# Kernel tuning notes

Hardware: AMD Instinct MI355X
Metric: run time of the kernel (lower is better)

## Reference

```python
import jax, jax.numpy as jnp
import numpy as np

D_MODEL = 192; D_INNER = 384; N_STATE = 16; D_CONV = 4; DT_RANK = 12; DEPTH = 24
PATCH = 16; STRIDE = 16; IMG = 128; EPS = 1e-5


def _ln(x, w, b):
    m = jnp.mean(x, -1, keepdims=True)
    v = jnp.mean((x - m) ** 2, -1, keepdims=True)
    return (x - m) * jax.lax.rsqrt(v + EPS) * w + b


def _mamba_dir(xz, cw, cb, xpw, dpw, dpb, Alog, Dv):
    # xz: (B, L, 2*d_inner); one direction of the bidirectional Mamba mixer
    xp, z = jnp.split(xz, 2, axis=-1)               # (B,L,di) each
    xc = jnp.transpose(xp, (0, 2, 1))               # (B,di,L)
    xc = jnp.pad(xc, ((0, 0), (0, 0), (D_CONV - 1, 0)))  # causal pad
    xc = jax.lax.conv_general_dilated(
        xc, cw, (1,), 'VALID',
        dimension_numbers=('NCH', 'OIH', 'NCH'),
        feature_group_count=D_INNER) + cb[None, :, None]
    u = jax.nn.silu(jnp.transpose(xc, (0, 2, 1)))   # (B,L,di)
    dbl = u @ xpw.T                                  # (B,L,dt_rank+2N)
    dt, Bm, Cm = jnp.split(dbl, [DT_RANK, DT_RANK + N_STATE], axis=-1)
    dt = jax.nn.softplus(dt @ dpw.T + dpb)           # (B,L,di)
    A = -jnp.exp(Alog)                               # (di,N)
    dA = jnp.exp(dt[..., None] * A)                  # (B,L,di,N)
    dBu = (dt * u)[..., None] * Bm[:, :, None, :]    # (B,L,di,N)

    def comb(c1, c2):
        a1, b1 = c1
        a2, b2 = c2
        return a1 * a2, a2 * b1 + b2

    _, h = jax.lax.associative_scan(comb, (dA, dBu), axis=1)
    y = jnp.einsum('bldn,bln->bld', h, Cm) + u * Dv
    return y * jax.nn.silu(z)


def _forward(x, patch_w, patch_b, ln_w, ln_b, in_w,
             cf_w, cf_b, xpf_w, dtf_w, dtf_b, Alog_f, D_f,
             cbk_w, cbk_b, xpb_w, dtb_w, dtb_b, Alog_b, D_b,
             out_w, nf_w, nf_b, head_w, head_b):
    B = x.shape[0]
    p = jax.lax.conv_general_dilated(
        x, patch_w, (STRIDE,) * 3, 'VALID',
        dimension_numbers=('NCDHW', 'OIDHW', 'NCDHW')) + patch_b[None, :, None, None, None]
    hidden = p.reshape(B, D_MODEL, -1).transpose(0, 2, 1)  # (B, L=512, D)
    residual = jnp.zeros_like(hidden)

    xs = (ln_w, ln_b, in_w, cf_w, cf_b, xpf_w, dtf_w, dtf_b, Alog_f, D_f,
          cbk_w, cbk_b, xpb_w, dtb_w, dtb_b, Alog_b, D_b, out_w)

    def step(carry, pl):
        hidden, residual = carry
        (lw, lb, iw, cfw, cfb, xpf, dwf, dbf, Af, Dfv,
         cbw, cbb, xpb, dwb, dbb, Ab, Dbv, ow) = pl
        residual = residual + hidden
        hn = _ln(residual, lw, lb)
        xz = hn @ iw.T                               # (B,L,2di)
        yf = _mamba_dir(xz, cfw, cfb, xpf, dwf, dbf, Af, Dfv)
        yb = jnp.flip(_mamba_dir(jnp.flip(xz, 1), cbw, cbb, xpb, dwb, dbb, Ab, Dbv), 1)
        hidden = (yf + yb) @ ow.T
        return (hidden, residual), None

    (hidden, residual), _ = jax.lax.scan(step, (hidden, residual), xs)
    final = _ln(residual + hidden, nf_w, nf_b)
    feat = final[:, -1, :]                           # final_pool_type='none' -> last token
    return feat @ head_w.T + head_b


def setup_inputs() -> dict:
    key = jax.random.key(0)
    ks = jax.random.split(key, 16)
    rn = lambda k, s, sc=0.02: jax.random.normal(k, s, jnp.float32) * sc
    d = {}
    d['x'] = jax.random.normal(ks[0], (1, 1, IMG, IMG, IMG), jnp.float32)
    d['patch_w'] = rn(ks[1], (D_MODEL, 1, PATCH, PATCH, PATCH), 0.05)
    d['patch_b'] = jnp.zeros((D_MODEL,), jnp.float32)
    d['ln_w'] = jnp.ones((DEPTH, D_MODEL), jnp.float32)
    d['ln_b'] = jnp.zeros((DEPTH, D_MODEL), jnp.float32)
    d['in_w'] = rn(ks[2], (DEPTH, 2 * D_INNER, D_MODEL))
    d['cf_w'] = rn(ks[3], (DEPTH, D_INNER, 1, D_CONV), 0.2)
    d['cf_b'] = jnp.zeros((DEPTH, D_INNER), jnp.float32)
    d['xpf_w'] = rn(ks[4], (DEPTH, DT_RANK + 2 * N_STATE, D_INNER))
    d['dtf_w'] = rn(ks[5], (DEPTH, D_INNER, DT_RANK), 0.1)
    d['dtf_b'] = jnp.full((DEPTH, D_INNER), -4.6, jnp.float32)  # softplus -> dt~0.01
    d['Alog_f'] = jnp.log(jnp.broadcast_to(jnp.arange(1, N_STATE + 1, dtype=jnp.float32), (DEPTH, D_INNER, N_STATE)))
    d['D_f'] = jnp.ones((DEPTH, D_INNER), jnp.float32)
    d['cbk_w'] = rn(ks[6], (DEPTH, D_INNER, 1, D_CONV), 0.2)
    d['cbk_b'] = jnp.zeros((DEPTH, D_INNER), jnp.float32)
    d['xpb_w'] = rn(ks[7], (DEPTH, DT_RANK + 2 * N_STATE, D_INNER))
    d['dtb_w'] = rn(ks[8], (DEPTH, D_INNER, DT_RANK), 0.1)
    d['dtb_b'] = jnp.full((DEPTH, D_INNER), -4.6, jnp.float32)
    d['Alog_b'] = jnp.log(jnp.broadcast_to(jnp.arange(1, N_STATE + 1, dtype=jnp.float32), (DEPTH, D_INNER, N_STATE)))
    d['D_b'] = jnp.ones((DEPTH, D_INNER), jnp.float32)
    d['out_w'] = rn(ks[9], (DEPTH, D_MODEL, D_INNER))
    d['nf_w'] = jnp.ones((D_MODEL,), jnp.float32)
    d['nf_b'] = jnp.zeros((D_MODEL,), jnp.float32)
    d['head_w'] = rn(ks[10], (2, D_MODEL))
    d['head_b'] = jnp.zeros((2,), jnp.float32)
    return d


def reference(x, patch_w, patch_b, ln_w, ln_b, in_w,
              cf_w, cf_b, xpf_w, dtf_w, dtf_b, Alog_f, D_f,
              cbk_w, cbk_b, xpb_w, dtb_w, dtb_b, Alog_b, D_b,
              out_w, nf_w, nf_b, head_w, head_b):
    return _forward(x, patch_w, patch_b, ln_w, ln_b, in_w,
                    cf_w, cf_b, xpf_w, dtf_w, dtf_b, Alog_f, D_f,
                    cbk_w, cbk_b, xpb_w, dtb_w, dtb_b, Alog_b, D_b,
                    out_w, nf_w, nf_b, head_w, head_b)
```

## Files before the change

### kernel.cpp

```cpp
#include <hip/hip_runtime.h>
#include <hip/hip_bf16.h>

#define D_MODEL 192
#define D_INNER 384
#define N_STATE 16
#define DT_RANK 12
#define DEPTH 24
#define SEQ 512
#define NCHUNK 8
#define CLEN 64
#define TS 68
#define AS 33
#define PART_STRIDE (SEQ * D_MODEL)
#define USTR (SEQ * D_INNER)
#define KSPLIT 16
#define NBLK 1024
#define FSTR 32
#define XZSTR (SEQ * 2 * D_INNER)
#define CHSTR (2 * NCHUNK * D_INNER * N_STATE)
#define GEN_OFF   1024
#define SCANR_OFF 1056
#define AFLAG_OFF 1440
#define BFLAG_OFF 1952
#define YFLAG_OFF 2976

typedef __hip_bfloat16 bf16;
typedef unsigned short u16;
typedef unsigned long long u64;

__device__ __forceinline__ float silu_f(float x) { return x / (1.f + __expf(-x)); }
__device__ __forceinline__ float softplus_f(float x) {
    return (x > 20.f) ? x : log1pf(__expf(x));
}
__device__ __forceinline__ float bf2f(unsigned u) {
    return __uint_as_float(u << 16);
}
__device__ __forceinline__ u16 f2bu(float f) {
    bf16 b = __float2bfloat16(f);
    return *reinterpret_cast<u16*>(&b);
}

__device__ __forceinline__ float aload(const float* p) {
    return __hip_atomic_load(p, __ATOMIC_RELAXED, __HIP_MEMORY_SCOPE_AGENT);
}
__device__ __forceinline__ void astore(float* p, float v) {
    __hip_atomic_store(p, v, __ATOMIC_RELAXED, __HIP_MEMORY_SCOPE_AGENT);
}
__device__ __forceinline__ unsigned aloadu(const unsigned* p) {
    return __hip_atomic_load(p, __ATOMIC_RELAXED, __HIP_MEMORY_SCOPE_AGENT);
}
__device__ __forceinline__ void astoreu(unsigned* p, unsigned v) {
    __hip_atomic_store(p, v, __ATOMIC_RELAXED, __HIP_MEMORY_SCOPE_AGENT);
}
__device__ __forceinline__ float2 aload2(const float* p) {
    const u64 v = __hip_atomic_load((const u64*)p, __ATOMIC_RELAXED, __HIP_MEMORY_SCOPE_AGENT);
    return make_float2(__uint_as_float((unsigned)v), __uint_as_float((unsigned)(v >> 32)));
}
__device__ __forceinline__ void astore2(float* p, float x, float y) {
    const u64 v = (u64)__float_as_uint(x) | ((u64)__float_as_uint(y) << 32);
    __hip_atomic_store((u64*)p, v, __ATOMIC_RELAXED, __HIP_MEMORY_SCOPE_AGENT);
}
__device__ __forceinline__ float4 aload4v(const float* p) {
    const float2 a = aload2(p), b = aload2(p + 2);
    return make_float4(a.x, a.y, b.x, b.y);
}
__device__ __forceinline__ float4 aload_bf4(const u16* p) {
    const u64 v = __hip_atomic_load((const u64*)p, __ATOMIC_RELAXED, __HIP_MEMORY_SCOPE_AGENT);
    return make_float4(bf2f((unsigned)(v & 0xffffu)),
                       bf2f((unsigned)((v >> 16) & 0xffffu)),
                       bf2f((unsigned)((v >> 32) & 0xffffu)),
                       bf2f((unsigned)(v >> 48)));
}
__device__ __forceinline__ void astore_bf4(u16* p, float a, float b, float c, float d) {
    const u64 v = (u64)f2bu(a) | ((u64)f2bu(b) << 16)
                | ((u64)f2bu(c) << 32) | ((u64)f2bu(d) << 48);
    __hip_atomic_store((u64*)p, v, __ATOMIC_RELAXED, __HIP_MEMORY_SCOPE_AGENT);
}

template<typename T> __device__ __forceinline__ float ld(const void* p, long i) {
    return ((const float*)p)[i];
}
template<> __device__ __forceinline__ float ld<bf16>(const void* p, long i) {
    return bf2f(((const u16*)p)[i]);
}
template<typename T> __device__ __forceinline__ float4 ld4(const void* p, long i) {
    return *(const float4*)((const float*)p + i);
}
template<> __device__ __forceinline__ float4 ld4<bf16>(const void* p, long i) {
    const ushort4 v = *(const ushort4*)((const u16*)p + i);
    return make_float4(bf2f(v.x), bf2f(v.y), bf2f(v.z), bf2f(v.w));
}
template<typename T> __device__ __forceinline__ void st(void* p, int i, float v) {
    ((float*)p)[i] = v;
}
template<> __device__ __forceinline__ void st<bf16>(void* p, int i, float v) {
    ((bf16*)p)[i] = __float2bfloat16(v);
}
__device__ __forceinline__ float dot4(const float4& a, const float4& b) {
    return a.x * b.x + a.y * b.y + a.z * b.z + a.w * b.w;
}
__device__ __forceinline__ void ld8b(const u16* p, float4& a, float4& b) {
    const uint4 u = *(const uint4*)p;
    a.x = bf2f(u.x & 0xffffu); a.y = bf2f(u.x >> 16);
    a.z = bf2f(u.y & 0xffffu); a.w = bf2f(u.y >> 16);
    b.x = bf2f(u.z & 0xffffu); b.y = bf2f(u.z >> 16);
    b.z = bf2f(u.w & 0xffffu); b.w = bf2f(u.w >> 16);
}
__device__ __forceinline__ float4 ld4b(const u16* p) {
    const uint2 u = *(const uint2*)p;
    return make_float4(bf2f(u.x & 0xffffu), bf2f(u.x >> 16),
                       bf2f(u.y & 0xffffu), bf2f(u.y >> 16));
}

__device__ __forceinline__ void post_flag(unsigned* fl, unsigned v, int tid) {
    asm volatile("s_waitcnt vmcnt(0)" ::: "memory");
    __syncthreads();
    if (tid == 0) astoreu(fl, v);
}
__device__ __forceinline__ void wait_flag(const unsigned* fl, unsigned v) {
    int spins = 0;
    while (aloadu(fl) < v) {
        if (++spins > (1 << 20)) break;
        __builtin_amdgcn_s_sleep(1);
    }
}

__device__ __forceinline__ void gbar(unsigned* bar, unsigned target, bool fence) {
    asm volatile("s_waitcnt vmcnt(0)" ::: "memory");
    __syncthreads();
    const int bid = blockIdx.x, tid = threadIdx.x;
    unsigned* gen0 = bar + GEN_OFF * FSTR;
    if (tid == 0) {
        if (fence) __threadfence();
        astoreu(&bar[bid * FSTR], target);
    }
    if (bid == 0) {
        int spins = 0;
        for (;;) {
            const unsigned va = aloadu(&bar[tid * FSTR]);
            const unsigned vb = aloadu(&bar[(tid + 256) * FSTR]);
            const unsigned vc = aloadu(&bar[(tid + 512) * FSTR]);
            const unsigned vd = aloadu(&bar[(tid + 768) * FSTR]);
            const bool ok = (va >= target) && (vb >= target) && (vc >= target) && (vd >= target);
            if (__syncthreads_and(ok)) break;
            if (++spins > (1 << 20)) break;
            __builtin_amdgcn_s_sleep(1);
        }
        if (tid == 0) astoreu(gen0, target);
    } else if (tid == 0) {
        int spins = 0;
        if (bid < 32) {
            while (aloadu(gen0) < target) {
                if (++spins > (1 << 20)) break;
                __builtin_amdgcn_s_sleep(2);
            }
            astoreu(&gen0[bid * FSTR], target);
        } else {
            unsigned* rl = &gen0[(bid >> 5) * FSTR];
            while (aloadu(rl) < target) {
                if (++spins > (1 << 20)) break;
                __builtin_amdgcn_s_sleep(2);
            }
        }
    }
    if (fence && tid == 0) __threadfence();
    __syncthreads();
}

__device__ void cvtB(const void* s, u16* d, long n, long g, long str, int isb) {
    if (isb) {
        const u16* p = (const u16*)s;
        for (long i = g * 4; i < n; i += str * 4) *(ushort4*)(d + i) = *(const ushort4*)(p + i);
    } else {
        const float* p = (const float*)s;
        for (long i = g * 4; i < n; i += str * 4) {
            const float4 v = *(const float4*)(p + i);
            ushort4 o; o.x = f2bu(v.x); o.y = f2bu(v.y); o.z = f2bu(v.z); o.w = f2bu(v.w);
            *(ushort4*)(d + i) = o;
        }
    }
}
__device__ void cvtF(const void* s, float* d, long n, long g, long str, int isb) {
    if (isb) {
        const u16* p = (const u16*)s;
        for (long i = g * 4; i < n; i += str * 4) {
            const ushort4 v = *(const ushort4*)(p + i);
            *(float4*)(d + i) = make_float4(bf2f(v.x), bf2f(v.y), bf2f(v.z), bf2f(v.w));
        }
    } else {
        const float* p = (const float*)s;
        for (long i = g * 4; i < n; i += str * 4) *(float4*)(d + i) = *(const float4*)(p + i);
    }
}
__device__ void cvtNA(const void* s, float* d, long n, long g, long str, int isb) {
    if (isb) {
        const u16* p = (const u16*)s;
        for (long i = g * 4; i < n; i += str * 4) {
            const ushort4 v = *(const ushort4*)(p + i);
            *(float4*)(d + i) = make_float4(-__expf(bf2f(v.x)), -__expf(bf2f(v.y)),
                                            -__expf(bf2f(v.z)), -__expf(bf2f(v.w)));
        }
    } else {
        const float* p = (const float*)s;
        for (long i = g * 4; i < n; i += str * 4) {
            const float4 v = *(const float4*)(p + i);
            *(float4*)(d + i) = make_float4(-__expf(v.x), -__expf(v.y), -__expf(v.z), -__expf(v.w));
        }
    }
}

template<typename T>
__device__ void final_phase(int tid, const float* res, const u16* yB, const void* ow,
                            const void* nw, const void* nb, const void* hw, const void* hb,
                            void* out, float* syf, float* f, float* red) {
    for (int j = tid; j < 96; j += 256) {
        const int q = j * 4;
        const float4 vf = aload_bf4(&yB[(long)511 * D_INNER + q]);
        const float4 vb = aload_bf4(&yB[(long)USTR + 511 * D_INNER + q]);
        *(float4*)&syf[q] = make_float4(vf.x + vb.x, vf.y + vb.y, vf.z + vb.z, vf.w + vb.w);
    }
    __syncthreads();
    float v = 0.f;
    if (tid < D_MODEL) {
        float acc = 0.f;
        const long wrow = (long)(DEPTH - 1) * D_MODEL * D_INNER + (long)tid * D_INNER;
        for (int k = 0; k < D_INNER; k += 4)
            acc += dot4(ld4<T>(ow, wrow + k), *(const float4*)&syf[k]);
        v = aload(&res[511 * D_MODEL + tid]) + acc;
    }
    float s = v;
    #pragma unroll
    for (int o = 32; o > 0; o >>= 1) s += __shfl_down(s, o, 64);
    if ((tid & 63) == 0 && tid < D_MODEL) red[tid >> 6] = s;
    __syncthreads();
    const float mean = (red[0] + red[1] + red[2]) * (1.f / D_MODEL);
    const float d = (tid < D_MODEL) ? (v - mean) : 0.f;
    float s2 = d * d;
    #pragma unroll
    for (int o = 32; o > 0; o >>= 1) s2 += __shfl_down(s2, o, 64);
    if ((tid & 63) == 0 && tid < D_MODEL) red[3 + (tid >> 6)] = s2;
    __syncthreads();
    const float var = (red[3] + red[4] + red[5]) * (1.f / D_MODEL);
    if (tid < D_MODEL)
        f[tid] = d * rsqrtf(var + 1e-5f) * ld<T>(nw, tid) + ld<T>(nb, tid);
    __syncthreads();
    if (tid < 2) {
        float a2 = ld<T>(hb, tid);
        for (int c = 0; c < D_MODEL; ++c) a2 += f[c] * ld<T>(hw, tid * D_MODEL + c);
        st<T>(out, tid, a2);
    }
}

struct MegaArgs {
    const void *x, *pw, *pb, *lnw, *lnb, *inw, *cfw, *cfb, *xpfw, *dtfw, *dtfb, *Af, *Dfv;
    const void *cbw, *cbb, *xpbw, *dtbw, *dtbb, *Ab, *Dbv, *ow, *nfw, *nfb, *hw, *hb;
    void* out;
    unsigned* bar;
    float *hidC, *res0, *res1, *dbl, *dt, *chunkH, *chunkP;
    u16 *xzB, *uB, *yB;
    float *lnwF, *lnbF, *cbfF, *cbbF, *dtbfF, *dtbbF, *negAfF, *negAbF, *DfF, *DbF, *pbF;
    u16 *inwB, *owB, *xB, *pwB, *xpwfB, *xpwbB, *dtwfB, *dtwbB, *cwfB, *cwbB;
};

__global__ void init_kernel(unsigned* bar) {
    const int i = blockIdx.x * 256 + threadIdx.x;
    ((uint4*)bar)[i] = make_uint4(0, 0, 0, 0);
}

__global__ void __launch_bounds__(256, 4) mega_kernel(MegaArgs a) {
    __shared__ float smem[6144];
    const int bid = blockIdx.x;
    const int tid = threadIdx.x;
    unsigned* bar = a.bar;
    unsigned* scanR = a.bar + SCANR_OFF * FSTR;
    unsigned* aflag = a.bar + AFLAG_OFF * FSTR;
    unsigned* bflag = a.bar + BFLAG_OFF * FSTR;
    unsigned* yflag = a.bar + YFLAG_OFF * FSTR;
    unsigned gen_ctr = 0;
    const int isb = (((const unsigned*)a.lnw)[0] != 0x3F800000u);

    {
        const long g = (long)bid * 256 + tid;
        const long str = (long)NBLK * 256;
        cvtB(a.inw,  a.inwB,  3538944, g, str, isb);
        cvtB(a.ow,   a.owB,   1769472, g, str, isb);
        cvtB(a.x,    a.xB,    2097152, g, str, isb);
        cvtB(a.pw,   a.pwB,    786432, g, str, isb);
        cvtB(a.xpfw, a.xpwfB,  405504, g, str, isb);
        cvtB(a.xpbw, a.xpwbB,  405504, g, str, isb);
        cvtB(a.dtfw, a.dtwfB,  110592, g, str, isb);
        cvtB(a.dtbw, a.dtwbB,  110592, g, str, isb);
        cvtB(a.cfw,  a.cwfB,    36864, g, str, isb);
        cvtB(a.cbw,  a.cwbB,    36864, g, str, isb);
        cvtF(a.lnw,  a.lnwF,     4608, g, str, isb);
        cvtF(a.lnb,  a.lnbF,     4608, g, str, isb);
        cvtF(a.cfb,  a.cbfF,     9216, g, str, isb);
        cvtF(a.cbb,  a.cbbF,     9216, g, str, isb);
        cvtF(a.dtfb, a.dtbfF,    9216, g, str, isb);
        cvtF(a.dtbb, a.dtbbF,    9216, g, str, isb);
        cvtF(a.pb,   a.pbF,       192, g, str, isb);
        cvtNA(a.Af,  a.negAfF,  147456, g, str, isb);
        cvtNA(a.Ab,  a.negAbF,  147456, g, str, isb);
        cvtF(a.Dfv,  a.DfF,      9216, g, str, isb);
        cvtF(a.Dbv,  a.DbF,      9216, g, str, isb);
    }
    gbar(bar, ++gen_ctr, true);

    if (bid < 768) {
        float* As_ = smem;
        float* Ws  = smem + 1056;
        const int ty = tid >> 4, tx = tid & 15;
        const int unit = bid;
        {
            const int mt = unit & 15, nt = (unit >> 4) % 3, ks = unit / 48;
            const int m0 = mt * 32, n0 = nt * 64, kk0 = ks * 256;
            float acc[2][4] = {};
            for (int kk = kk0; kk < kk0 + 256; kk += 32) {
                for (int e = tid; e < 1024; e += 256) {
                    const int m = e >> 5, k = e & 31;
                    const int kid = kk + k, t = m0 + m;
                    const int dz = kid >> 8, dy = (kid >> 4) & 15, dx = kid & 15;
                    const int pz = t >> 6, py = (t >> 3) & 7, px = t & 7;
                    As_[k * AS + m] = bf2f(a.xB[(long)(pz * 16 + dz) * 16384 + (py * 16 + dy) * 128 + (px * 16 + dx)]);
                }
                for (int e = tid; e < 2048; e += 256) {
                    const int n = e >> 5, k = e & 31;
                    Ws[k * TS + n] = bf2f(a.pwB[(long)(n0 + n) * 4096 + kk + k]);
                }
                __syncthreads();
                #pragma unroll 8
                for (int k = 0; k < 32; ++k) {
                    const float a0 = As_[k * AS + ty * 2];
                    const float a1 = As_[k * AS + ty * 2 + 1];
                    const float4 w4 = *(const float4*)&Ws[k * TS + tx * 4];
                    acc[0][0] += a0 * w4.x; acc[0][1] += a0 * w4.y;
                    acc[0][2] += a0 * w4.z; acc[0][3] += a0 * w4.w;
                    acc[1][0] += a1 * w4.x; acc[1][1] += a1 * w4.y;
                    acc[1][2] += a1 * w4.z; acc[1][3] += a1 * w4.w;
                }
                __syncthreads();
            }
            float* C = a.hidC + (long)ks * PART_STRIDE;
            #pragma unroll
            for (int i = 0; i < 2; ++i) {
                float4 o4 = make_float4(acc[i][0], acc[i][1], acc[i][2], acc[i][3]);
                if (ks == 0) {
                    o4.x += a.pbF[n0 + tx * 4 + 0];
                    o4.y += a.pbF[n0 + tx * 4 + 1];
                    o4.z += a.pbF[n0 + tx * 4 + 2];
                    o4.w += a.pbF[n0 + tx * 4 + 3];
                }
                astore2(&C[(m0 + ty * 2 + i) * D_MODEL + n0 + tx * 4], o4.x, o4.y);
                astore2(&C[(m0 + ty * 2 + i) * D_MODEL + n0 + tx * 4 + 2], o4.z, o4.w);
            }
        }
    }
    gbar(bar, ++gen_ctr, false);

    const int ch = tid >> 4, np = tid & 15;
    float* sU  = smem;
    float* sDT = smem + 1024;
    float* sBC = smem + 2048;
    float* sZ  = smem + 4096;
    float* sY  = smem + 5120;

    for (int l = 0; l < DEPTH; ++l) {
        const int first = (l == 0);
        const unsigned lv = (unsigned)(l + 1);
        const int par = l & 1;
        u16* xzP = a.xzB + (long)par * XZSTR;
        u16* uP  = a.uB  + (long)par * (2 * USTR);
        float* dtP = a.dt + (long)par * (2 * USTR);
        float* dbG = a.dbl + (long)par * (2 * SEQ * 44);
        float* chH = a.chunkH + (long)par * CHSTR;
        float* chPb = a.chunkP + (long)par * CHSTR;
        const float* resIn = par ? a.res1 : a.res0;
        float* resOut      = par ? a.res0 : a.res1;

        if (bid < 512) {
            const int t = bid;
            if (par) {
                if (tid < 48) {
                    const int dd = tid / 24, dg = tid - dd * 24;
                    const int cf = t >> 6;
                    const int cbk = (511 - t) >> 6;
                    const int cc = dd ? cbk : cf;
                    wait_flag(&yflag[((dd * NCHUNK + cc) * 24 + dg) * FSTR], (unsigned)l);
                }
                __syncthreads();
            }
            float* sy  = smem;
            float* lnS = smem + 384;
            float* hnS = smem + 576;
            float* xzS = smem + 768;
            if (!first && tid < 96) {
                const int q4 = tid * 4;
                const long o = (long)t * D_INNER + q4;
                const float4 vf = aload_bf4(&a.yB[o]);
                const float4 vb = aload_bf4(&a.yB[(long)USTR + o]);
                *(float4*)&sy[q4] = make_float4(vf.x + vb.x, vf.y + vb.y, vf.z + vb.z, vf.w + vb.w);
            }
            __syncthreads();
            if (tid < D_MODEL) {
                float acc;
                if (first) {
                    float s = 0.f;
                    #pragma unroll
                    for (int sp = 0; sp < KSPLIT; ++sp)
                        s += aload(&a.hidC[(long)sp * PART_STRIDE + t * D_MODEL + tid]);
                    acc = s;
                } else {
                    acc = 0.f;
                    const u16* wr = a.owB + (long)(l - 1) * D_MODEL * D_INNER + (long)tid * D_INNER;
                    for (int k = 0; k < D_INNER; k += 8) {
                        float4 va, vb;
                        ld8b(wr + k, va, vb);
                        acc += dot4(va, *(const float4*)&sy[k]) + dot4(vb, *(const float4*)&sy[k + 4]);
                    }
                }
                const float rv = acc + (first ? 0.f : aload(&resIn[t * D_MODEL + tid]));
                lnS[tid] = rv;
                astore(&resOut[t * D_MODEL + tid], rv);
            }
            __syncthreads();
            {
                const int w = tid >> 6, lane = tid & 63;
                if (w == 0) {
                    const float v0 = lnS[lane];
                    const float v1 = lnS[lane + 64];
                    const float v2 = lnS[lane + 128];
                    float s = v0 + v1 + v2;
                    #pragma unroll
                    for (int o = 32; o > 0; o >>= 1) s += __shfl_xor(s, o, 64);
                    const float mean = s * (1.f / D_MODEL);
                    const float d0 = v0 - mean, d1 = v1 - mean, d2 = v2 - mean;
                    float s2 = d0 * d0 + d1 * d1 + d2 * d2;
                    #pragma unroll
                    for (int o = 32; o > 0; o >>= 1) s2 += __shfl_xor(s2, o, 64);
                    const float rstd = rsqrtf(s2 * (1.f / D_MODEL) + 1e-5f);
                    hnS[lane]       = d0 * rstd * a.lnwF[l * D_MODEL + lane]       + a.lnbF[l * D_MODEL + lane];
                    hnS[lane + 64]  = d1 * rstd * a.lnwF[l * D_MODEL + lane + 64]  + a.lnbF[l * D_MODEL + lane + 64];
                    hnS[lane + 128] = d2 * rstd * a.lnwF[l * D_MODEL + lane + 128] + a.lnbF[l * D_MODEL + lane + 128];
                }
            }
            __syncthreads();
            float accD[3] = {};
            const u16* w0 = a.inwB + (long)l * 2 * D_INNER * D_MODEL;
            for (int k = 0; k < D_MODEL; k += 8) {
                #pragma unroll
                for (int r = 0; r < 3; ++r) {
                    float4 va, vb;
                    ld8b(w0 + (long)(tid + r * 256) * D_MODEL + k, va, vb);
                    accD[r] += dot4(va, *(const float4*)&hnS[k])
                             + dot4(vb, *(const float4*)&hnS[k + 4]);
                }
            }
            #pragma unroll
            for (int r = 0; r < 3; ++r) xzS[tid + r * 256] = accD[r];
            __syncthreads();
            if (tid < 192) {
                const int q = tid * 4;
                const float* s = &xzS[q];
                astore_bf4(&xzP[(long)t * 2 * D_INNER + q], s[0], s[1], s[2], s[3]);
            }
            post_flag(&aflag[t * FSTR], lv, tid);
        }

        {
            const int dir = bid >> 9, t = bid & 511;
            int lo, hi;
            if (dir == 0) { lo = t >= 3 ? t - 3 : 0; hi = t; }
            else { lo = 508 - t >= 0 ? 508 - t : 0; hi = 511 - t; }
            if (tid <= hi - lo) wait_flag(&aflag[(lo + tid) * FSTR], lv);
            __syncthreads();

            float* su   = smem;
            float* dblP = smem + 384;
            float* dblS = smem + 472;
            const u16* cwB   = dir ? a.cwbB  : a.cwfB;
            const float* cbF = dir ? a.cbbF  : a.cbfF;
            const u16* xpwB  = dir ? a.xpwbB : a.xpwfB;
            const u16* dtwB  = dir ? a.dtwbB : a.dtwfB;
            const float* dtbF = dir ? a.dtbbF : a.dtbfF;
            u16* ub = uP + (long)dir * USTR;
            if (tid < 96) {
                const int q4 = tid * 4;
                float4 wA, wB2, wC, wD;
                ld8b(cwB + (long)(l * D_INNER + q4) * 4, wA, wB2);
                ld8b(cwB + (long)(l * D_INNER + q4) * 4 + 8, wC, wD);
                const float cw0[4] = {wA.x, wA.y, wA.z, wA.w};
                const float cw1[4] = {wB2.x, wB2.y, wB2.z, wB2.w};
                const float cw2[4] = {wC.x, wC.y, wC.z, wC.w};
                const float cw3[4] = {wD.x, wD.y, wD.z, wD.w};
                float4 acc = *(const float4*)&cbF[l * D_INNER + q4];
                #pragma unroll
                for (int k = 0; k < 4; ++k) {
                    const int ii = t + k - 3;
                    if (ii >= 0) {
                        const int src = dir ? (511 - ii) : ii;
                        const float4 xq = aload_bf4(&xzP[(long)src * 2 * D_INNER + q4]);
                        acc.x += xq.x * cw0[k]; acc.y += xq.y * cw1[k];
                        acc.z += xq.z * cw2[k]; acc.w += xq.w * cw3[k];
                    }
                }
                const float u0 = silu_f(acc.x), u1 = silu_f(acc.y);
                const float u2 = silu_f(acc.z), u3 = silu_f(acc.w);
                *(float4*)&su[q4] = make_float4(u0, u1, u2, u3);
                astore_bf4(&ub[(long)t * D_INNER + q4], u0, u1, u2, u3);
            }
            __syncthreads();
            if (tid < 88) {
                const int half = tid / 44, out = tid - half * 44;
                const u16* wr = xpwB + (long)(l * 44 + out) * D_INNER;
                const int k0 = half * 192;
                float acc = 0.f;
                for (int k = k0; k < k0 + 192; k += 8) {
                    float4 va, vb;
                    ld8b(wr + k, va, vb);
                    acc += dot4(va, *(const float4*)&su[k]) + dot4(vb, *(const float4*)&su[k + 4]);
                }
                dblP[half * 44 + out] = acc;
            }
            __syncthreads();
            if (tid < 44) {
                const float s = dblP[tid] + dblP[44 + tid];
                dblS[tid] = s;
                astore(&dbG[(long)dir * SEQ * 44 + (long)t * 44 + tid], s);
            }
            __syncthreads();
            float* dtp = dtP + (long)dir * USTR;
            if (tid < 192) {
                const int d2 = tid * 2;
                const u16* wr = dtwB + (long)(l * D_INNER + d2) * DT_RANK;
                float4 A0, B0; ld8b(wr, A0, B0);
                const float4 C0 = ld4b(wr + 8);
                float4 A1, B1; ld8b(wr + 12, A1, B1);
                const float4 C1 = ld4b(wr + 20);
                const float4 ds0 = *(const float4*)&dblS[0];
                const float4 ds1 = *(const float4*)&dblS[4];
                const float4 ds2 = *(const float4*)&dblS[8];
                const float acc0 = dtbF[l * D_INNER + d2]
                    + dot4(A0, ds0) + dot4(B0, ds1) + dot4(C0, ds2);
                const float acc1 = dtbF[l * D_INNER + d2 + 1]
                    + dot4(A1, ds0) + dot4(B1, ds1) + dot4(C1, ds2);
                astore2(&dtp[(long)t * D_INNER + d2], softplus_f(acc0), softplus_f(acc1));
            }
            post_flag(&bflag[bid * FSTR], lv, tid);
        }

        if (bid < 384) {
            const int dg = bid % 24, chunk = (bid / 24) & 7, dir2 = bid / 192;
            const int t0s = chunk * CLEN;
            if (tid < 64) wait_flag(&bflag[(dir2 * 512 + t0s + tid) * FSTR], lv);
            __syncthreads();
            const int d0 = dg * 16, d = d0 + ch;
            const u16* ubq  = uP + (long)dir2 * USTR;
            const float* dtp = dtP + (long)dir2 * USTR;
            const float* db  = dbG + (long)dir2 * SEQ * 44;
            {
                const int t = tid >> 2, dl4 = (tid & 3) * 4;
                const int tg = t0s + t;
                const long base = (long)tg * D_INNER + d0 + dl4;
                *(float4*)&sU[t * 16 + dl4]  = aload_bf4(&ubq[base]);
                *(float4*)&sDT[t * 16 + dl4] = aload4v(&dtp[base]);
                const int out_l = dir2 ? (511 - tg) : tg;
                *(float4*)&sZ[t * 16 + dl4] = aload_bf4(&xzP[(long)out_l * 2 * D_INNER + D_INNER + d0 + dl4]);
            }
            for (int i = tid; i < 512; i += 256) {
                const int t = i >> 3, j4 = (i & 7) * 4;
                *(float4*)&sBC[t * 32 + j4] = aload4v(&db[(long)(t0s + t) * 44 + DT_RANK + j4]);
            }
            const float* negA = dir2 ? a.negAbF : a.negAfF;
            const float Areg = negA[(long)(l * D_INNER + d) * N_STATE + np];
            const float Dval = (dir2 ? a.DbF : a.DfF)[l * D_INNER + d];
            __syncthreads();
            float h = 0.f, dts = 0.f;
            for (int t = 0; t < CLEN; ++t) {
                const float dtv = sDT[t * 16 + ch];
                h = __expf(dtv * Areg) * h + (dtv * sU[t * 16 + ch]) * sBC[t * 32 + np];
                dts += dtv;
            }
            const long cb2 = ((long)(dir2 * NCHUNK + chunk) * D_INNER + d) * N_STATE + np;
            astore(&chH[cb2], h);
            astore(&chPb[cb2], __expf(Areg * dts));
            post_flag(&scanR[((dir2 * NCHUNK + chunk) * 24 + dg) * FSTR], lv, tid);
            if (tid < chunk) wait_flag(&scanR[((dir2 * NCHUNK + tid) * 24 + dg) * FSTR], lv);
            __syncthreads();
            float hs[NCHUNK - 1], ps[NCHUNK - 1];
            #pragma unroll
            for (int c = 0; c < NCHUNK - 1; ++c) {
                if (c < chunk) {
                    const long cbb = ((long)(dir2 * NCHUNK + c) * D_INNER + d) * N_STATE + np;
                    hs[c] = aload(&chH[cbb]);
                    ps[c] = aload(&chPb[cbb]);
                }
            }
            float h0 = 0.f;
            #pragma unroll
            for (int c = 0; c < NCHUNK - 1; ++c)
                if (c < chunk) h0 = ps[c] * h0 + hs[c];
            h = h0;
            for (int t = 0; t < CLEN; ++t) {
                const float dtv = sDT[t * 16 + ch];
                const float uv = sU[t * 16 + ch];
                h = __expf(dtv * Areg) * h + (dtv * uv) * sBC[t * 32 + np];
                float part = h * sBC[t * 32 + 16 + np];
                part += __shfl_xor(part, 1, 64);
                part += __shfl_xor(part, 2, 64);
                part += __shfl_xor(part, 4, 64);
                part += __shfl_xor(part, 8, 64);
                if (np == 0)
                    sY[t * 16 + ch] = (part + uv * Dval) * silu_f(sZ[t * 16 + ch]);
            }
            __syncthreads();
            {
                const int t = tid >> 2, dl4 = (tid & 3) * 4;
                const int tg = t0s + t;
                const int out_l = dir2 ? (511 - tg) : tg;
                u16* yb = a.yB + (long)dir2 * USTR;
                const float* s = &sY[t * 16 + dl4];
                astore_bf4(&yb[(long)out_l * D_INNER + d0 + dl4], s[0], s[1], s[2], s[3]);
            }
            post_flag(&yflag[((dir2 * NCHUNK + chunk) * 24 + dg) * FSTR], lv, tid);
        }
        if (par) gbar(bar, ++gen_ctr, false);
    }

    if (bid == 0) {
        float* syf = smem;
        float* f   = smem + 384;
        float* red = smem + 576;
        if (isb) final_phase<bf16>(tid, a.res0, a.yB, a.ow, a.nfw, a.nfb, a.hw, a.hb, a.out, syf, f, red);
        else     final_phase<float>(tid, a.res0, a.yB, a.ow, a.nfw, a.nfb, a.hw, a.hb, a.out, syf, f, red);
    }
}

extern "C" void kernel_launch(void* const* d_in, const int* in_sizes, int n_in,
                              void* d_out, int out_size, void* d_ws, size_t ws_size,
                              hipStream_t stream) {
    (void)in_sizes; (void)n_in; (void)out_size; (void)ws_size;
    const void* x    = d_in[0];
    const void* pw   = d_in[1];
    const void* pb   = d_in[2];
    const void* lnw  = d_in[3];
    const void* lnb  = d_in[4];
    const void* inw  = d_in[5];
    const void* cfw  = d_in[6];
    const void* cfb  = d_in[7];
    const void* xpfw = d_in[8];
    const void* dtfw = d_in[9];
    const void* dtfb = d_in[10];
    const void* Af   = d_in[11];
    const void* Dfv  = d_in[12];
    const void* cbw  = d_in[13];
    const void* cbb  = d_in[14];
    const void* xpbw = d_in[15];
    const void* dtbw = d_in[16];
    const void* dtbb = d_in[17];
    const void* Ab   = d_in[18];
    const void* Dbv  = d_in[19];
    const void* ow   = d_in[20];
    const void* nfw  = d_in[21];
    const void* nfb  = d_in[22];
    const void* hw   = d_in[23];
    const void* hb   = d_in[24];

    unsigned* bar = (unsigned*)d_ws;
    float* w = (float*)((char*)d_ws + 524288);
    float* hidC   = w;  w += KSPLIT * PART_STRIDE;
    float* res0   = w;  w += PART_STRIDE;
    float* res1   = w;  w += PART_STRIDE;
    float* dbl    = w;  w += 2 * 2 * SEQ * 44;
    float* dt     = w;  w += 2 * 2 * USTR;
    float* chunkH = w;  w += 2 * CHSTR;
    float* chunkP = w;  w += 2 * CHSTR;
    float* lnwF = w;  w += 4608;
    float* lnbF = w;  w += 4608;
    float* cbfF = w;  w += 9216;
    float* cbbF = w;  w += 9216;
    float* dtbfF = w; w += 9216;
    float* dtbbF = w; w += 9216;
    float* negAfF = w; w += 147456;
    float* negAbF = w; w += 147456;
    float* DfF = w;   w += 9216;
    float* DbF = w;   w += 9216;
    float* pbF = w;   w += 192;
    u16* b = (u16*)w;
    u16* xzB = b;  b += 2 * XZSTR;
    u16* uB  = b;  b += 2 * 2 * USTR;
    u16* yB  = b;  b += 2 * USTR;
    u16* inwB  = b;  b += 3538944;
    u16* owB   = b;  b += 1769472;
    u16* xB    = b;  b += 2097152;
    u16* pwB   = b;  b += 786432;
    u16* xpwfB = b;  b += 405504;
    u16* xpwbB = b;  b += 405504;
    u16* dtwfB = b;  b += 110592;
    u16* dtwbB = b;  b += 110592;
    u16* cwfB  = b;  b += 36864;
    u16* cwbB  = b;  b += 36864;

    MegaArgs ma;
    ma.x = x; ma.pw = pw; ma.pb = pb; ma.lnw = lnw; ma.lnb = lnb; ma.inw = inw;
    ma.cfw = cfw; ma.cfb = cfb; ma.xpfw = xpfw; ma.dtfw = dtfw; ma.dtfb = dtfb;
    ma.Af = Af; ma.Dfv = Dfv; ma.cbw = cbw; ma.cbb = cbb; ma.xpbw = xpbw;
    ma.dtbw = dtbw; ma.dtbb = dtbb; ma.Ab = Ab; ma.Dbv = Dbv; ma.ow = ow;
    ma.nfw = nfw; ma.nfb = nfb; ma.hw = hw; ma.hb = hb; ma.out = d_out;
    ma.bar = bar;
    ma.hidC = hidC; ma.res0 = res0; ma.res1 = res1; ma.dbl = dbl; ma.dt = dt;
    ma.chunkH = chunkH; ma.chunkP = chunkP;
    ma.xzB = xzB; ma.uB = uB; ma.yB = yB;
    ma.lnwF = lnwF; ma.lnbF = lnbF; ma.cbfF = cbfF; ma.cbbF = cbbF;
    ma.dtbfF = dtbfF; ma.dtbbF = dtbbF; ma.negAfF = negAfF; ma.negAbF = negAbF;
    ma.DfF = DfF; ma.DbF = DbF; ma.pbF = pbF;
    ma.inwB = inwB; ma.owB = owB; ma.xB = xB; ma.pwB = pwB;
    ma.xpwfB = xpwfB; ma.xpwbB = xpwbB; ma.dtwfB = dtwfB; ma.dtwbB = dtwbB;
    ma.cwfB = cwfB; ma.cwbB = cwbB;

    init_kernel<<<128, 256, 0, stream>>>(bar);
    mega_kernel<<<NBLK, 256, 0, stream>>>(ma);
}
```

Measured before the change: 1.817 ms.

## Halve persistent grid and fuse both scan directions into one block per token

The persistent megakernel grid drops from 1024 to 512 blocks with two blocks per CU instead of four. Each block now does the in-projection for its token and then computes conv, x-proj and dt for both directions itself, reusing its own xz row from shared memory. The separate per-direction block stage and its flag array are merged into one combined flag. This cuts grid-barrier traffic and flag handoffs, but each block does more serial work and fewer waves are available to hide latency.

```diff
diff --git a/kernel.cpp b/kernel.cpp
--- a/kernel.cpp
+++ b/kernel.cpp
@@ -14,15 +14,15 @@
 #define PART_STRIDE (SEQ * D_MODEL)
 #define USTR (SEQ * D_INNER)
 #define KSPLIT 16
-#define NBLK 1024
+#define NBLK 512
 #define FSTR 32
 #define XZSTR (SEQ * 2 * D_INNER)
 #define CHSTR (2 * NCHUNK * D_INNER * N_STATE)
-#define GEN_OFF   1024
-#define SCANR_OFF 1056
-#define AFLAG_OFF 1440
-#define BFLAG_OFF 1952
-#define YFLAG_OFF 2976
+#define GEN_OFF    512
+#define SCANR_OFF  528
+#define AFLAG_OFF  912
+#define ABFLAG_OFF 1424
+#define YFLAG_OFF  1936
 
 typedef __hip_bfloat16 bf16;
 typedef unsigned short u16;
@@ -139,9 +139,7 @@
         for (;;) {
             const unsigned va = aloadu(&bar[tid * FSTR]);
             const unsigned vb = aloadu(&bar[(tid + 256) * FSTR]);
-            const unsigned vc = aloadu(&bar[(tid + 512) * FSTR]);
-            const unsigned vd = aloadu(&bar[(tid + 768) * FSTR]);
-            const bool ok = (va >= target) && (vb >= target) && (vc >= target) && (vd >= target);
+            const bool ok = (va >= target) && (vb >= target);
             if (__syncthreads_and(ok)) break;
             if (++spins > (1 << 20)) break;
             __builtin_amdgcn_s_sleep(1);
@@ -149,12 +147,17 @@
         if (tid == 0) astoreu(gen0, target);
     } else if (tid == 0) {
         int spins = 0;
-        if (bid < 32) {
+        if (bid < 16) {
             while (aloadu(gen0) < target) {
                 if (++spins > (1 << 20)) break;
                 __builtin_amdgcn_s_sleep(2);
             }
             astoreu(&gen0[bid * FSTR], target);
+        } else if (bid < 32) {
+            while (aloadu(gen0) < target) {
+                if (++spins > (1 << 20)) break;
+                __builtin_amdgcn_s_sleep(2);
+            }
         } else {
             unsigned* rl = &gen0[(bid >> 5) * FSTR];
             while (aloadu(rl) < target) {
@@ -267,15 +270,15 @@
     ((uint4*)bar)[i] = make_uint4(0, 0, 0, 0);
 }
 
-__global__ void __launch_bounds__(256, 4) mega_kernel(MegaArgs a) {
+__global__ void __launch_bounds__(256, 2) mega_kernel(MegaArgs a) {
     __shared__ float smem[6144];
     const int bid = blockIdx.x;
     const int tid = threadIdx.x;
     unsigned* bar = a.bar;
-    unsigned* scanR = a.bar + SCANR_OFF * FSTR;
-    unsigned* aflag = a.bar + AFLAG_OFF * FSTR;
-    unsigned* bflag = a.bar + BFLAG_OFF * FSTR;
-    unsigned* yflag = a.bar + YFLAG_OFF * FSTR;
+    unsigned* scanR  = a.bar + SCANR_OFF * FSTR;
+    unsigned* aflag  = a.bar + AFLAG_OFF * FSTR;
+    unsigned* abflag = a.bar + ABFLAG_OFF * FSTR;
+    unsigned* yflag  = a.bar + YFLAG_OFF * FSTR;
     unsigned gen_ctr = 0;
     const int isb = (((const unsigned*)a.lnw)[0] != 0x3F800000u);
 
@@ -306,12 +309,11 @@
     }
     gbar(bar, ++gen_ctr, true);
 
-    if (bid < 768) {
+    {
         float* As_ = smem;
         float* Ws  = smem + 1056;
         const int ty = tid >> 4, tx = tid & 15;
-        const int unit = bid;
-        {
+        for (int unit = bid; unit < 768; unit += NBLK) {
             const int mt = unit & 15, nt = (unit >> 4) % 3, ks = unit / 48;
             const int m0 = mt * 32, n0 = nt * 64, kk0 = ks * 256;
             float acc[2][4] = {};
@@ -377,7 +379,7 @@
         const float* resIn = par ? a.res1 : a.res0;
         float* resOut      = par ? a.res0 : a.res1;
 
-        if (bid < 512) {
+        {
             const int t = bid;
             if (par) {
                 if (tid < 48) {
@@ -464,27 +466,20 @@
                 astore_bf4(&xzP[(long)t * 2 * D_INNER + q], s[0], s[1], s[2], s[3]);
             }
             post_flag(&aflag[t * FSTR], lv, tid);
-        }
-
-        {
-            const int dir = bid >> 9, t = bid & 511;
-            int lo, hi;
-            if (dir == 0) { lo = t >= 3 ? t - 3 : 0; hi = t; }
-            else { lo = 508 - t >= 0 ? 508 - t : 0; hi = 511 - t; }
-            if (tid <= hi - lo) wait_flag(&aflag[(lo + tid) * FSTR], lv);
+
+            if (tid < 7) {
+                const int tt = t - 3 + tid;
+                if (tt >= 0 && tt <= 511 && tt != t) wait_flag(&aflag[tt * FSTR], lv);
+            }
             __syncthreads();
 
             float* su   = smem;
-            float* dblP = smem + 384;
-            float* dblS = smem + 472;
-            const u16* cwB   = dir ? a.cwbB  : a.cwfB;
-            const float* cbF = dir ? a.cbbF  : a.cbfF;
-            const u16* xpwB  = dir ? a.xpwbB : a.xpwfB;
-            const u16* dtwB  = dir ? a.dtwbB : a.dtwfB;
-            const float* dtbF = dir ? a.dtbbF : a.dtbfF;
-            u16* ub = uP + (long)dir * USTR;
-            if (tid < 96) {
-                const int q4 = tid * 4;
+            float* dblP = smem + 1536;
+            float* dblS = smem + 1712;
+            if (tid < 192) {
+                const int dirm = tid / 96, q4 = (tid - dirm * 96) * 4;
+                const u16* cwB   = dirm ? a.cwbB  : a.cwfB;
+                const float* cbF = dirm ? a.cbbF  : a.cbfF;
                 float4 wA, wB2, wC, wD;
                 ld8b(cwB + (long)(l * D_INNER + q4) * 4, wA, wB2);
                 ld8b(cwB + (long)(l * D_INNER + q4) * 4 + 8, wC, wD);
@@ -492,66 +487,81 @@
                 const float cw1[4] = {wB2.x, wB2.y, wB2.z, wB2.w};
                 const float cw2[4] = {wC.x, wC.y, wC.z, wC.w};
                 const float cw3[4] = {wD.x, wD.y, wD.z, wD.w};
+                const int tok = dirm ? (511 - t) : t;
                 float4 acc = *(const float4*)&cbF[l * D_INNER + q4];
                 #pragma unroll
                 for (int k = 0; k < 4; ++k) {
-                    const int ii = t + k - 3;
+                    const int ii = tok + k - 3;
                     if (ii >= 0) {
-                        const int src = dir ? (511 - ii) : ii;
-                        const float4 xq = aload_bf4(&xzP[(long)src * 2 * D_INNER + q4]);
+                        const int src = dirm ? (511 - ii) : ii;
+                        float4 xq;
+                        if (src == t) xq = *(const float4*)&xzS[q4];
+                        else          xq = aload_bf4(&xzP[(long)src * 2 * D_INNER + q4]);
                         acc.x += xq.x * cw0[k]; acc.y += xq.y * cw1[k];
                         acc.z += xq.z * cw2[k]; acc.w += xq.w * cw3[k];
                     }
                 }
                 const float u0 = silu_f(acc.x), u1 = silu_f(acc.y);
                 const float u2 = silu_f(acc.z), u3 = silu_f(acc.w);
-                *(float4*)&su[q4] = make_float4(u0, u1, u2, u3);
-                astore_bf4(&ub[(long)t * D_INNER + q4], u0, u1, u2, u3);
-            }
-            __syncthreads();
-            if (tid < 88) {
-                const int half = tid / 44, out = tid - half * 44;
+                *(float4*)&su[dirm * 384 + q4] = make_float4(u0, u1, u2, u3);
+                astore_bf4(&uP[(long)dirm * USTR + (long)tok * D_INNER + q4], u0, u1, u2, u3);
+            }
+            __syncthreads();
+            if (tid < 176) {
+                const int dirm = tid / 88, r = tid - dirm * 88;
+                const int half = r / 44, out = r - half * 44;
+                const u16* xpwB = dirm ? a.xpwbB : a.xpwfB;
                 const u16* wr = xpwB + (long)(l * 44 + out) * D_INNER;
                 const int k0 = half * 192;
                 float acc = 0.f;
                 for (int k = k0; k < k0 + 192; k += 8) {
                     float4 va, vb;
                     ld8b(wr + k, va, vb);
-                    acc += dot4(va, *(const float4*)&su[k]) + dot4(vb, *(const float4*)&su[k + 4]);
-                }
-                dblP[half * 44 + out] = acc;
-            }
-            __syncthreads();
-            if (tid < 44) {
-                const float s = dblP[tid] + dblP[44 + tid];
-                dblS[tid] = s;
-                astore(&dbG[(long)dir * SEQ * 44 + (long)t * 44 + tid], s);
-            }
-            __syncthreads();
-            float* dtp = dtP + (long)dir * USTR;
-            if (tid < 192) {
-                const int d2 = tid * 2;
+                    acc += dot4(va, *(const float4*)&su[dirm * 384 + k])
+                         + dot4(vb, *(const float4*)&su[dirm * 384 + k + 4]);
+                }
+                dblP[dirm * 88 + half * 44 + out] = acc;
+            }
+            __syncthreads();
+            if (tid < 88) {
+                const int dirm = tid / 44, out = tid - dirm * 44;
+                const float s = dblP[dirm * 88 + out] + dblP[dirm * 88 + 44 + out];
+                dblS[dirm * 44 + out] = s;
+                const int tok = dirm ? (511 - t) : t;
+                astore(&dbG[(long)dirm * SEQ * 44 + (long)tok * 44 + out], s);
+            }
+            __syncthreads();
+            for (int j = tid; j < 384; j += 256) {
+                const int dirm = j / 192, d2 = (j - dirm * 192) * 2;
+                const u16* dtwB  = dirm ? a.dtwbB : a.dtwfB;
+                const float* dtbF = dirm ? a.dtbbF : a.dtbfF;
+                const int tok = dirm ? (511 - t) : t;
                 const u16* wr = dtwB + (long)(l * D_INNER + d2) * DT_RANK;
                 float4 A0, B0; ld8b(wr, A0, B0);
                 const float4 C0 = ld4b(wr + 8);
                 float4 A1, B1; ld8b(wr + 12, A1, B1);
                 const float4 C1 = ld4b(wr + 20);
-                const float4 ds0 = *(const float4*)&dblS[0];
-                const float4 ds1 = *(const float4*)&dblS[4];
-                const float4 ds2 = *(const float4*)&dblS[8];
+                const float4 ds0 = *(const float4*)&dblS[dirm * 44];
+                const float4 ds1 = *(const float4*)&dblS[dirm * 44 + 4];
+                const float4 ds2 = *(const float4*)&dblS[dirm * 44 + 8];
                 const float acc0 = dtbF[l * D_INNER + d2]
                     + dot4(A0, ds0) + dot4(B0, ds1) + dot4(C0, ds2);
                 const float acc1 = dtbF[l * D_INNER + d2 + 1]
                     + dot4(A1, ds0) + dot4(B1, ds1) + dot4(C1, ds2);
-                astore2(&dtp[(long)t * D_INNER + d2], softplus_f(acc0), softplus_f(acc1));
-            }
-            post_flag(&bflag[bid * FSTR], lv, tid);
+                astore2(&dtP[(long)dirm * USTR + (long)tok * D_INNER + d2],
+                        softplus_f(acc0), softplus_f(acc1));
+            }
+            post_flag(&abflag[t * FSTR], lv, tid);
         }
 
         if (bid < 384) {
             const int dg = bid % 24, chunk = (bid / 24) & 7, dir2 = bid / 192;
             const int t0s = chunk * CLEN;
-            if (tid < 64) wait_flag(&bflag[(dir2 * 512 + t0s + tid) * FSTR], lv);
+            if (tid < 64) {
+                const int tg = t0s + tid;
+                const int pb = dir2 ? (511 - tg) : tg;
+                wait_flag(&abflag[pb * FSTR], lv);
+            }
             __syncthreads();
             const int d0 = dg * 16, d = d0 + ch;
             const u16* ubq  = uP + (long)dir2 * USTR;
```

Measured after the change: 1.802 ms, median of 2. No clear change (-0.8%).
